# Performance work log

Hardware: AMD Instinct MI355X
Metric: run time of the kernel (lower is better)

The kernel has to match this reference:

```python
import jax, jax.numpy as jnp
import numpy as np

N_NODES = 100000
N_EDGES = 3200000
D_IN = 128
D_OUT = 128


def setup_inputs() -> dict:
    key = jax.random.key(0)
    k1, k2, k3, k4, k5 = jax.random.split(key, 5)
    x = jax.random.normal(k1, (N_NODES, D_IN), dtype=jnp.float32)
    adj_rows = jax.random.randint(k2, (N_EDGES,), 0, N_NODES, dtype=jnp.int64)
    adj_cols = jax.random.randint(k3, (N_EDGES,), 0, N_NODES, dtype=jnp.int64)
    adj_vals = jax.random.uniform(k4, (N_EDGES,), dtype=jnp.float32)
    # torch Linear weight has shape (dim_out, dim_in)
    W = jax.random.normal(k5, (D_OUT, D_IN), dtype=jnp.float32) * (1.0 / np.sqrt(D_IN))
    return {"x": x, "adj_rows": adj_rows, "adj_cols": adj_cols, "adj_vals": adj_vals, "W": W}


def reference(x, adj_rows, adj_cols, adj_vals, W):
    # h = Linear(x) with no bias: x @ W^T  -> [N, D_OUT]
    h = x @ W.T
    # sparse.mm(adjacency, h): out[r] = sum_e vals[e] * h[cols[e]] for edges with rows[e]==r
    msgs = adj_vals[:, None] * h[adj_cols]           # [E, D_OUT]
    agg = jax.ops.segment_sum(msgs, adj_rows, num_segments=N_NODES)
    return jax.nn.relu(agg)
```

## Files before the change

### kernel.cpp

```cpp
#include <hip/hip_runtime.h>
#include <stdint.h>

typedef unsigned short u16;
typedef unsigned int u32;
typedef unsigned long long u64;
typedef __attribute__((ext_vector_type(8))) short short8;
typedef __attribute__((ext_vector_type(4))) float floatx4;

#define DIM 128
#define DIM2 64
#define NBK 2048
#define NB_SH 6
#define AGG_NB 64
#define AGG_CAP 2560
#define SC_C 4096

__device__ __forceinline__ u32 f32_to_bf16_rne(float f) {
  u32 u = __float_as_uint(f);
  u32 r = u + 0x7fffu + ((u >> 16) & 1u);
  return r >> 16;
}
__device__ __forceinline__ float bf16_to_f32(u32 u) { return __uint_as_float(u << 16); }
__device__ __forceinline__ u32 pack2bf16(float a, float b) {
  return f32_to_bf16_rne(a) | (f32_to_bf16_rne(b) << 16);
}

union FragU {
  u32 d[4];
  short8 s;
};

__global__ __launch_bounds__(256) void gemm_mfma(const float* __restrict__ x,
                                                 const float* __restrict__ W,
                                                 u16* __restrict__ h, int N) {
  __shared__ u32 Wl[DIM * DIM2];
  int tid = threadIdx.x;
#pragma unroll
  for (int i = 0; i < 8; ++i) {
    int ga = tid + 256 * i;
    int o = ga >> 4, g = ga & 15;
    const float* src = W + (size_t)o * DIM + g * 8;
    floatx4 f0 = *(const floatx4*)src;
    floatx4 f1 = *(const floatx4*)(src + 4);
    int slot = (g + o) & 15;
    u32* dst = &Wl[o * DIM2 + slot * 4];
    dst[0] = pack2bf16(f0.x, f0.y);
    dst[1] = pack2bf16(f0.z, f0.w);
    dst[2] = pack2bf16(f1.x, f1.y);
    dst[3] = pack2bf16(f1.z, f1.w);
  }
  __syncthreads();

  int lane = tid & 63;
  int wave = tid >> 6;
  int nodeBase = (blockIdx.x * 4 + wave) * 16;
  if (nodeBase >= N) return;
  int m = lane & 15;
  int kg = lane >> 4;

  short8 a[4];
  const float* xr = x + (size_t)(nodeBase + m) * DIM + kg * 8;
#pragma unroll
  for (int kt = 0; kt < 4; ++kt) {
    floatx4 f0 = *(const floatx4*)(xr + kt * 32);
    floatx4 f1 = *(const floatx4*)(xr + kt * 32 + 4);
    FragU fu;
    fu.d[0] = pack2bf16(f0.x, f0.y);
    fu.d[1] = pack2bf16(f0.z, f0.w);
    fu.d[2] = pack2bf16(f1.x, f1.y);
    fu.d[3] = pack2bf16(f1.z, f1.w);
    a[kt] = fu.s;
  }

#pragma unroll
  for (int ot = 0; ot < 8; ++ot) {
    int o = ot * 16 + m;
    floatx4 acc = {0.f, 0.f, 0.f, 0.f};
#pragma unroll
    for (int kt = 0; kt < 4; ++kt) {
      int slot = (kt * 4 + kg + o) & 15;
      short8 b = *(short8*)&Wl[o * DIM2 + slot * 4];
      acc = __builtin_amdgcn_mfma_f32_16x16x32_bf16(a[kt], b, acc, 0, 0, 0);
    }
#pragma unroll
    for (int r = 0; r < 4; ++r) {
      int node = nodeBase + kg * 4 + r;
      h[(size_t)node * DIM + ot * 16 + m] = (u16)f32_to_bf16_rne(acc[r]);
    }
  }
}

__global__ void zero_kernel(int* __restrict__ p, int n) {
  int i = blockIdx.x * blockDim.x + threadIdx.x;
  if (i < n) p[i] = 0;
}

__device__ __forceinline__ void scan2048(u32* cnt, u32* excl, u32* wtot) {
  int tid = threadIdx.x, lane = tid & 63, wave = tid >> 6;
  u32 c[8], sum = 0;
#pragma unroll
  for (int k = 0; k < 8; ++k) {
    c[k] = cnt[tid * 8 + k];
    sum += c[k];
  }
  u32 inc = sum;
#pragma unroll
  for (int d = 1; d < 64; d <<= 1) {
    u32 t = __shfl_up(inc, d, 64);
    if (lane >= d) inc += t;
  }
  if (lane == 63) wtot[wave] = inc;
  __syncthreads();
  u32 wbase = 0;
  for (int w = 0; w < wave; ++w) wbase += wtot[w];
  u32 run = wbase + inc - sum;
#pragma unroll
  for (int k = 0; k < 8; ++k) {
    excl[tid * 8 + k] = run;
    run += c[k];
  }
  __syncthreads();
}

__global__ __launch_bounds__(256) void bucket_hist(const int* __restrict__ rows,
                                                   int* __restrict__ bhist, int E, int B) {
  __shared__ u32 hist[NBK];
  int tid = threadIdx.x;
  for (int b = tid; b < NBK; b += 256) hist[b] = 0;
  __syncthreads();
  int base = blockIdx.x * SC_C;
  for (int j = tid; j < SC_C; j += 256) {
    int e = base + j;
    if (e < E) atomicAdd(&hist[((u32)rows[e]) >> NB_SH], 1u);
  }
  __syncthreads();
  for (int b = tid; b < B; b += 256) {
    u32 c = hist[b];
    if (c) atomicAdd(&bhist[b], (int)c);
  }
}

__global__ __launch_bounds__(256) void bucket_scan(const int* __restrict__ bhist,
                                                   int* __restrict__ bbase,
                                                   int* __restrict__ bptr) {
  __shared__ u32 cnt[NBK], excl[NBK], wtot[4];
  int tid = threadIdx.x;
  for (int b = tid; b < NBK; b += 256) cnt[b] = (u32)bhist[b];
  __syncthreads();
  scan2048(cnt, excl, wtot);
  for (int b = tid; b < NBK; b += 256) {
    bbase[b] = (int)excl[b];
    bptr[b] = (int)excl[b];
  }
}

__global__ __launch_bounds__(256) void bin_scatter(const int* __restrict__ rows,
                                                   const int* __restrict__ cols,
                                                   const float* __restrict__ vals,
                                                   int* __restrict__ bptr,
                                                   u32* __restrict__ bcol,
                                                   u16* __restrict__ bval, int E) {
  __shared__ u32 hist[NBK];
  __shared__ u32 starts[NBK];
  __shared__ u32 gbase[NBK];
  __shared__ u32 wtot[4];
  __shared__ u32 s_lo[SC_C];
  __shared__ u16 s_val[SC_C];
  __shared__ u16 s_bkt[SC_C];
  int tid = threadIdx.x;
  int base = blockIdx.x * SC_C;
  int tot = min(SC_C, E - base);

  for (int b = tid; b < NBK; b += 256) hist[b] = 0;
  __syncthreads();
  for (int j = tid; j < tot; j += 256) {
    atomicAdd(&hist[((u32)rows[base + j]) >> NB_SH], 1u);
  }
  __syncthreads();
  scan2048(hist, starts, wtot);
  for (int b = tid; b < NBK; b += 256) {
    u32 c = hist[b];
    gbase[b] = c ? (u32)atomicAdd(&bptr[b], (int)c) : 0u;
    hist[b] = starts[b];
  }
  __syncthreads();
  for (int j = tid; j < tot; j += 256) {
    int e = base + j;
    u32 r = (u32)rows[e];
    u32 bk = r >> NB_SH;
    u32 p = atomicAdd(&hist[bk], 1u);
    s_lo[p] = ((r & 63u) << 26) | ((u32)cols[e] << 8);
    s_val[p] = (u16)f32_to_bf16_rne(vals[e]);
    s_bkt[p] = (u16)bk;
  }
  __syncthreads();
  for (int i = tid; i < tot; i += 256) {
    u32 bk = s_bkt[i];
    u32 d = gbase[bk] + ((u32)i - starts[bk]);
    bcol[d] = s_lo[i];
    bval[d] = s_val[i];
  }
}

__global__ __launch_bounds__(256) void agg_bucket(const int* __restrict__ bhist,
                                                  const int* __restrict__ bbase,
                                                  const u32* __restrict__ bcol,
                                                  const u16* __restrict__ bval,
                                                  const u32* __restrict__ h,
                                                  float* __restrict__ out, int N) {
  __shared__ u64 s_rec[AGG_CAP];
  __shared__ u32 cnt[AGG_NB], excl[AGG_NB], ptr[AGG_NB];
  int tid = threadIdx.x, lane = tid & 63, wave = tid >> 6;
  int b = blockIdx.x;
  int base = bbase[b], T = bhist[b];
  int nodeBase = b << NB_SH;
  int lane4 = lane * 4;
  const char* hb = (const char*)h;

  if (T <= AGG_CAP) {
    if (tid < AGG_NB) cnt[tid] = 0;
    __syncthreads();
    u32 rlo[10], rv[10];
#pragma unroll
    for (int k = 0; k < 10; ++k) {
      int j = tid + 256 * k;
      rlo[k] = 0;
      rv[k] = 0;
      if (j < T) {
        rlo[k] = bcol[base + j];
        rv[k] = bval[base + j];
        atomicAdd(&cnt[rlo[k] >> 26], 1u);
      }
    }
    __syncthreads();
    if (tid < 64) {
      u32 c = cnt[tid], inc = c;
#pragma unroll
      for (int d = 1; d < 64; d <<= 1) {
        u32 t = __shfl_up(inc, d, 64);
        if (lane >= d) inc += t;
      }
      excl[tid] = inc - c;
      ptr[tid] = inc - c;
    }
    __syncthreads();
#pragma unroll
    for (int k = 0; k < 10; ++k) {
      int j = tid + 256 * k;
      if (j < T) {
        u32 p = atomicAdd(&ptr[rlo[k] >> 26], 1u);
        s_rec[p] = ((u64)(rv[k] << 16) << 32) | rlo[k];
      }
    }
    __syncthreads();
    int wbeg = (int)excl[wave * 16];
    int wend = (int)ptr[wave * 16 + 15];
    float a0 = 0.f, a1 = 0.f;
    int curn = -1;
    for (int e = wbeg; e < wend; e += 8) {
      u32 lo8[8];
      float v8[8];
      u32 hd[8];
#pragma unroll
      for (int g = 0; g < 8; ++g) {
        int ee = e + g;
        bool act = ee < wend;
        u64 r = s_rec[act ? ee : (wend - 1)];
        lo8[g] = (u32)r;
        v8[g] = act ? __uint_as_float((u32)(r >> 32)) : 0.f;
      }
#pragma unroll
      for (int g = 0; g < 8; ++g) {
        hd[g] = *(const u32*)(hb + ((lo8[g] & 0x01FFFF00u) + lane4));
      }
#pragma unroll
      for (int g = 0; g < 8; ++g) {
        int nid = __builtin_amdgcn_readfirstlane((int)(lo8[g] >> 26));
        if (nid != curn) {
          if (curn >= 0) {
            float2 o = make_float2(fmaxf(a0, 0.f), fmaxf(a1, 0.f));
            *(float2*)(out + (size_t)(nodeBase + curn) * DIM + 2 * lane) = o;
          }
          curn = nid;
          a0 = 0.f;
          a1 = 0.f;
        }
        float v = v8[g];
        a0 += v * bf16_to_f32(hd[g] & 0xffffu);
        a1 += v * bf16_to_f32(hd[g] >> 16);
      }
    }
    if (curn >= 0) {
      float2 o = make_float2(fmaxf(a0, 0.f), fmaxf(a1, 0.f));
      *(float2*)(out + (size_t)(nodeBase + curn) * DIM + 2 * lane) = o;
    }
    for (int nn = 0; nn < 16; ++nn) {
      int nl = wave * 16 + nn;
      int node = nodeBase + nl;
      if (cnt[nl] == 0 && node < N) {
        *(float2*)(out + (size_t)node * DIM + 2 * lane) = make_float2(0.f, 0.f);
      }
    }
  } else {
    for (int nn = 0; nn < 16; ++nn) {
      int nl = wave * 16 + nn;
      int node = nodeBase + nl;
      if (node >= N) continue;
      float a0 = 0.f, a1 = 0.f;
      for (int e = 0; e < T; ++e) {
        u32 lo = bcol[base + e];
        if ((int)(lo >> 26) == nl) {
          u32 d = *(const u32*)(hb + ((lo & 0x01FFFF00u) + lane4));
          float v = bf16_to_f32(bval[base + e]);
          a0 += v * bf16_to_f32(d & 0xffffu);
          a1 += v * bf16_to_f32(d >> 16);
        }
      }
      *(float2*)(out + (size_t)node * DIM + 2 * lane) =
          make_float2(fmaxf(a0, 0.f), fmaxf(a1, 0.f));
    }
  }
}

extern "C" void kernel_launch(void* const* d_in, const int* in_sizes, int n_in,
                              void* d_out, int out_size, void* d_ws, size_t ws_size,
                              hipStream_t stream) {
  const float* x    = (const float*)d_in[0];
  const int*   rows = (const int*)d_in[1];
  const int*   cols = (const int*)d_in[2];
  const float* vals = (const float*)d_in[3];
  const float* W    = (const float*)d_in[4];

  const int N = in_sizes[0] / DIM;
  const int E = in_sizes[1];
  const int B = (N + AGG_NB - 1) / AGG_NB;

  char* wsb = (char*)d_ws;
  size_t o = 0;
  u16* h = (u16*)wsb;                    o += (size_t)N * DIM * sizeof(u16);
  int* bhist = (int*)(wsb + o);          o += (size_t)NBK * 4;
  int* bbase = (int*)(wsb + o);          o += (size_t)NBK * 4;
  int* bptr  = (int*)(wsb + o);          o += (size_t)NBK * 4;
  u32* bcol  = (u32*)(wsb + o);          o += (size_t)E * 4;
  u16* bval  = (u16*)(wsb + o);          o += (size_t)E * 2;

  const int nsc = (E + SC_C - 1) / SC_C;

  zero_kernel<<<(NBK + 255) / 256, 256, 0, stream>>>(bhist, NBK);
  gemm_mfma<<<(N + 63) / 64, 256, 0, stream>>>(x, W, h, N);
  bucket_hist<<<nsc, 256, 0, stream>>>(rows, bhist, E, B);
  bucket_scan<<<1, 256, 0, stream>>>(bhist, bbase, bptr);
  bin_scatter<<<nsc, 256, 0, stream>>>(rows, cols, vals, bptr, bcol, bval, E);
  agg_bucket<<<B, 256, 0, stream>>>(bhist, bbase, bcol, bval, (const u32*)h,
                                    (float*)d_out, N);
}
```

Measured before the change: 361.9 us.

## Use persistent GEMM blocks and doubled scatter chunks with packed index records

The GEMM becomes persistent: a fixed grid of 256 blocks loops over node tiles, so each block converts W to bf16 into LDS once and reuses it across many tiles. The binning scatter now handles 8192 edges per block. Instead of staging col, value and bucket in shared memory, it stores one packed 32-bit record of bucket, local row and edge offset, then reads cols and vals straight from global memory in the write-out pass. This halves the number of scatter blocks and their global bucket-pointer atomics, and makes output runs per bucket longer. In exchange the cols and vals reads are now scattered, and the larger chunk uses more LDS, which may lower occupancy.

```diff
diff --git a/kernel.cpp b/kernel.cpp
--- a/kernel.cpp
+++ b/kernel.cpp
@@ -13,7 +13,8 @@
 #define NB_SH 6
 #define AGG_NB 64
 #define AGG_CAP 2560
-#define SC_C 4096
+#define SC_C 8192
+#define HIST_C 4096
 
 __device__ __forceinline__ u32 f32_to_bf16_rne(float f) {
   u32 u = __float_as_uint(f);
@@ -53,39 +54,43 @@
 
   int lane = tid & 63;
   int wave = tid >> 6;
-  int nodeBase = (blockIdx.x * 4 + wave) * 16;
-  if (nodeBase >= N) return;
   int m = lane & 15;
   int kg = lane >> 4;
-
-  short8 a[4];
-  const float* xr = x + (size_t)(nodeBase + m) * DIM + kg * 8;
-#pragma unroll
-  for (int kt = 0; kt < 4; ++kt) {
-    floatx4 f0 = *(const floatx4*)(xr + kt * 32);
-    floatx4 f1 = *(const floatx4*)(xr + kt * 32 + 4);
-    FragU fu;
-    fu.d[0] = pack2bf16(f0.x, f0.y);
-    fu.d[1] = pack2bf16(f0.z, f0.w);
-    fu.d[2] = pack2bf16(f1.x, f1.y);
-    fu.d[3] = pack2bf16(f1.z, f1.w);
-    a[kt] = fu.s;
-  }
-
-#pragma unroll
-  for (int ot = 0; ot < 8; ++ot) {
-    int o = ot * 16 + m;
-    floatx4 acc = {0.f, 0.f, 0.f, 0.f};
+  int ntile = (N + 63) >> 6;
+
+  for (int t = blockIdx.x; t < ntile; t += 256) {
+    int nodeBase = t * 64 + wave * 16;
+    if (nodeBase >= N) continue;
+
+    short8 a[4];
+    const float* xr = x + (size_t)(nodeBase + m) * DIM + kg * 8;
 #pragma unroll
     for (int kt = 0; kt < 4; ++kt) {
-      int slot = (kt * 4 + kg + o) & 15;
-      short8 b = *(short8*)&Wl[o * DIM2 + slot * 4];
-      acc = __builtin_amdgcn_mfma_f32_16x16x32_bf16(a[kt], b, acc, 0, 0, 0);
-    }
-#pragma unroll
-    for (int r = 0; r < 4; ++r) {
-      int node = nodeBase + kg * 4 + r;
-      h[(size_t)node * DIM + ot * 16 + m] = (u16)f32_to_bf16_rne(acc[r]);
+      floatx4 f0 = *(const floatx4*)(xr + kt * 32);
+      floatx4 f1 = *(const floatx4*)(xr + kt * 32 + 4);
+      FragU fu;
+      fu.d[0] = pack2bf16(f0.x, f0.y);
+      fu.d[1] = pack2bf16(f0.z, f0.w);
+      fu.d[2] = pack2bf16(f1.x, f1.y);
+      fu.d[3] = pack2bf16(f1.z, f1.w);
+      a[kt] = fu.s;
+    }
+
+#pragma unroll
+    for (int ot = 0; ot < 8; ++ot) {
+      int o = ot * 16 + m;
+      floatx4 acc = {0.f, 0.f, 0.f, 0.f};
+#pragma unroll
+      for (int kt = 0; kt < 4; ++kt) {
+        int slot = (kt * 4 + kg + o) & 15;
+        short8 b = *(short8*)&Wl[o * DIM2 + slot * 4];
+        acc = __builtin_amdgcn_mfma_f32_16x16x32_bf16(a[kt], b, acc, 0, 0, 0);
+      }
+#pragma unroll
+      for (int r = 0; r < 4; ++r) {
+        int node = nodeBase + kg * 4 + r;
+        h[(size_t)node * DIM + ot * 16 + m] = (u16)f32_to_bf16_rne(acc[r]);
+      }
     }
   }
 }
@@ -128,8 +133,8 @@
   int tid = threadIdx.x;
   for (int b = tid; b < NBK; b += 256) hist[b] = 0;
   __syncthreads();
-  int base = blockIdx.x * SC_C;
-  for (int j = tid; j < SC_C; j += 256) {
+  int base = blockIdx.x * HIST_C;
+  for (int j = tid; j < HIST_C; j += 256) {
     int e = base + j;
     if (e < E) atomicAdd(&hist[((u32)rows[e]) >> NB_SH], 1u);
   }
@@ -164,9 +169,7 @@
   __shared__ u32 starts[NBK];
   __shared__ u32 gbase[NBK];
   __shared__ u32 wtot[4];
-  __shared__ u32 s_lo[SC_C];
-  __shared__ u16 s_val[SC_C];
-  __shared__ u16 s_bkt[SC_C];
+  __shared__ u32 s_rec[SC_C];
   int tid = threadIdx.x;
   int base = blockIdx.x * SC_C;
   int tot = min(SC_C, E - base);
@@ -185,20 +188,20 @@
   }
   __syncthreads();
   for (int j = tid; j < tot; j += 256) {
-    int e = base + j;
-    u32 r = (u32)rows[e];
+    u32 r = (u32)rows[base + j];
     u32 bk = r >> NB_SH;
     u32 p = atomicAdd(&hist[bk], 1u);
-    s_lo[p] = ((r & 63u) << 26) | ((u32)cols[e] << 8);
-    s_val[p] = (u16)f32_to_bf16_rne(vals[e]);
-    s_bkt[p] = (u16)bk;
+    s_rec[p] = (bk << 19) | ((r & 63u) << 13) | (u32)j;
   }
   __syncthreads();
   for (int i = tid; i < tot; i += 256) {
-    u32 bk = s_bkt[i];
+    u32 rec = s_rec[i];
+    u32 bk = rec >> 19;
+    u32 nl = (rec >> 13) & 63u;
+    int e = base + (int)(rec & 8191u);
     u32 d = gbase[bk] + ((u32)i - starts[bk]);
-    bcol[d] = s_lo[i];
-    bval[d] = s_val[i];
+    bcol[d] = (nl << 26) | ((u32)cols[e] << 8);
+    bval[d] = (u16)f32_to_bf16_rne(vals[e]);
   }
 }
 
@@ -344,11 +347,12 @@
   u32* bcol  = (u32*)(wsb + o);          o += (size_t)E * 4;
   u16* bval  = (u16*)(wsb + o);          o += (size_t)E * 2;
 
+  const int nhist = (E + HIST_C - 1) / HIST_C;
   const int nsc = (E + SC_C - 1) / SC_C;
 
   zero_kernel<<<(NBK + 255) / 256, 256, 0, stream>>>(bhist, NBK);
-  gemm_mfma<<<(N + 63) / 64, 256, 0, stream>>>(x, W, h, N);
-  bucket_hist<<<nsc, 256, 0, stream>>>(rows, bhist, E, B);
+  gemm_mfma<<<256, 256, 0, stream>>>(x, W, h, N);
+  bucket_hist<<<nhist, 256, 0, stream>>>(rows, bhist, E, B);
   bucket_scan<<<1, 256, 0, stream>>>(bhist, bbase, bptr);
   bin_scatter<<<nsc, 256, 0, stream>>>(rows, cols, vals, bptr, bcol, bval, E);
   agg_bucket<<<B, 256, 0, stream>>>(bhist, bbase, bcol, bval, (const u32*)h,
```

New measurement: 344.9 us. 1.05x faster.
